# Performance work log

Measured on AMD Instinct MI355X. Metric: run time of the kernel, lower is better.

## Reference

```python
import jax, jax.numpy as jnp
import numpy as np
from jax import lax

EPS = 1e-5

def _conv(x, w, stride, padding):
    # x: NCHW, w: OIHW
    return lax.conv_general_dilated(
        x, w, window_strides=(stride, stride), padding=padding,
        dimension_numbers=("NCHW", "OIHW", "NCHW"))

def _bn(x, gamma, beta):
    # BatchNorm2d in training mode: batch statistics over (N, H, W)
    mean = jnp.mean(x, axis=(0, 2, 3), keepdims=True)
    var = jnp.var(x, axis=(0, 2, 3), keepdims=True)
    inv = lax.rsqrt(var + EPS)
    g = gamma.reshape(1, -1, 1, 1)
    b = beta.reshape(1, -1, 1, 1)
    return (x - mean) * inv * g + b

def setup_inputs() -> dict:
    key = jax.random.key(0)
    ks = jax.random.split(key, 5)
    B, Cin, H, W = 128, 64, 56, 56
    Cout = 128
    x = jax.random.normal(ks[0], (B, Cin, H, W), dtype=jnp.float32)
    w1 = jax.random.normal(ks[1], (Cout, Cin, 3, 3), dtype=jnp.float32) * 0.05
    w2 = jax.random.normal(ks[2], (Cout, Cout, 3, 3), dtype=jnp.float32) * 0.05
    wd = jax.random.normal(ks[3], (Cout, Cin, 1, 1), dtype=jnp.float32) * 0.05
    g1 = jnp.ones((Cout,), jnp.float32); b1 = jnp.zeros((Cout,), jnp.float32)
    g2 = jnp.ones((Cout,), jnp.float32); b2 = jnp.zeros((Cout,), jnp.float32)
    gd = jnp.ones((Cout,), jnp.float32); bd = jnp.zeros((Cout,), jnp.float32)
    return {"x": x, "w1": w1, "g1": g1, "b1": b1,
            "w2": w2, "g2": g2, "b2": b2,
            "wd": wd, "gd": gd, "bd": bd}

def reference(x, w1, g1, b1, w2, g2, b2, wd, gd, bd):
    stride = 2
    # conv1 (3x3, stride=2, 'same') -> BN -> ReLU
    out = _conv(x, w1, stride, "SAME")
    out = jax.nn.relu(_bn(out, g1, b1))
    # conv2 (3x3, stride=1, 'same') -> BN
    out = _conv(out, w2, 1, "SAME")
    out = _bn(out, g2, b2)
    # downsample identity: 1x1 conv stride=2 'valid' -> BN
    identity = _bn(_conv(x, wd, stride, "VALID"), gd, bd)
    return jax.nn.relu(out + identity)
```

## Files before the change

### kernel.cpp

```cpp
#include <hip/hip_runtime.h>

constexpr int B = 128, Cin = 64, H = 56, W = 56;
constexpr int Cout = 128, Ho = 28, Wo = 28;
constexpr int HW = Ho * Wo;
constexpr int NPIX = B * HW;
constexpr int NOUT = NPIX * Cout;
constexpr int NBLK = NPIX / 128;
constexpr float EPS_ = 1e-5f;
constexpr float CNT_ = (float)NPIX;

constexpr int HPX = 57, WPX = 57;
constexpr int HP1 = 30, WP1 = 30;

typedef __attribute__((ext_vector_type(8))) unsigned short u16x8;
typedef __attribute__((ext_vector_type(4))) unsigned short u16x4;
typedef __attribute__((ext_vector_type(8))) short bf16x8;
typedef __attribute__((ext_vector_type(4))) float f32x4;

__device__ inline float bf2f(unsigned short u) {
    union { unsigned int i; float f; } v; v.i = ((unsigned int)u) << 16; return v.f;
}
__device__ inline unsigned short f2bf(float f) {
    union { float f; unsigned int i; } v; v.f = f;
    return (unsigned short)((v.i + 0x7fffu + ((v.i >> 16) & 1u)) >> 16);
}

__device__ inline void gload16(const void* g, void* l) {
    __builtin_amdgcn_global_load_lds(
        (const __attribute__((address_space(1))) unsigned int*)g,
        (__attribute__((address_space(3))) unsigned int*)l, 16, 0, 0);
}

template<int STRIDE, int HP, int WP, int CIN, int KHW, bool OUTPAD, bool FUSE_DW>
__global__ __launch_bounds__(256) void k_conv_mfma(
        const unsigned short* __restrict__ xin,
        const unsigned short* __restrict__ wt,
        unsigned short* __restrict__ yout,
        float* __restrict__ part,
        const unsigned short* __restrict__ wtd,
        unsigned short* __restrict__ ydout,
        float* __restrict__ partd) {
    constexpr int KTOT = KHW * KHW * CIN;
    constexpr int NSTEP = KTOT / 32;
    constexpr int CSTEPS = CIN / 32;
    constexpr int RING = FUSE_DW ? 2 : 3;
    __shared__ unsigned short Alds[RING][128 * 32];
    __shared__ unsigned short Blds[RING][128 * 32];
    __shared__ unsigned short BdLds[FUSE_DW ? 2 * 128 * 32 : 4];
    __shared__ float lsum[4][64], lsq[4][64];
    const int tid = threadIdx.x, w = tid >> 6, l = tid & 63;
    const int wr = w >> 1, wc = w & 1;
    const int bid = (blockIdx.x & 7) * (NBLK / 8) + (blockIdx.x >> 3);
    const int p0 = bid * 128;
    const char* xb = (const char*)xin;
    const char* wb = (const char*)wt;
    const char* wdb = (const char*)wtd;

    const int sslot = ((l & 3) ^ ((l >> 3) & 3)) * 16;
    int gA[2], gB[2], gBd[2], lofs[2];
    #pragma unroll
    for (int i = 0; i < 2; ++i) {
        int row = w * 32 + i * 16 + (l >> 2);
        int p = p0 + row;
        int n = p / HW, rr = p % HW;
        int oh = rr / Wo, ow = rr % Wo;
        gA[i] = (((n * HP + oh * STRIDE) * WP + ow * STRIDE) * CIN) * 2 + sslot;
        gB[i] = (row * KTOT) * 2 + sslot;
        gBd[i] = row * 128 + sslot;
        lofs[i] = row * 64 + (l & 3) * 16;
    }

    f32x4 acc[4][4], accd[4][4];
    #pragma unroll
    for (int m = 0; m < 4; ++m)
        #pragma unroll
        for (int n = 0; n < 4; ++n) {
            acc[m][n] = (f32x4){0.f, 0.f, 0.f, 0.f};
            if constexpr (FUSE_DW) accd[m][n] = (f32x4){0.f, 0.f, 0.f, 0.f};
        }

    auto STAGE = [&](int s, int buf) {
        const int seg = s / CSTEPS;
        const int c0 = (s % CSTEPS) * 32;
        const int kh = seg / KHW, kw = seg % KHW;
        const int koffA = (((kh * WP + kw) * CIN) + c0) * 2;
        const int koffB = s * 64;
        gload16(xb + gA[0] + koffA, (char*)Alds[buf] + lofs[0]);
        gload16(xb + gA[1] + koffA, (char*)Alds[buf] + lofs[1]);
        gload16(wb + gB[0] + koffB, (char*)Blds[buf] + lofs[0]);
        gload16(wb + gB[1] + koffB, (char*)Blds[buf] + lofs[1]);
    };

    const int rswz = ((l >> 4) ^ ((l >> 1) & 3)) * 16;

    if constexpr (FUSE_DW) {
        #pragma unroll
        for (int s = 0; s < 2; ++s)
            #pragma unroll
            for (int i = 0; i < 2; ++i)
                gload16(wdb + gBd[i] + s * 64, (char*)BdLds + s * 8192 + lofs[i]);
    }
    STAGE(0, 0);
    if constexpr (!FUSE_DW) STAGE(1, 1);

    for (int s = 0; s < NSTEP; ++s) {
        const int cur = s % RING;
        if constexpr (FUSE_DW) {
            if (s + 1 < NSTEP) {
                STAGE(s + 1, (s + 1) % RING);
                asm volatile("s_waitcnt vmcnt(4)" ::: "memory");
            } else {
                asm volatile("s_waitcnt vmcnt(0)" ::: "memory");
            }
        } else {
            if (s + 2 < NSTEP) {
                STAGE(s + 2, (s + 2) % RING);
                asm volatile("s_waitcnt vmcnt(8)" ::: "memory");
            } else if (s + 1 < NSTEP) {
                asm volatile("s_waitcnt vmcnt(4)" ::: "memory");
            } else {
                asm volatile("s_waitcnt vmcnt(0)" ::: "memory");
            }
        }
        __builtin_amdgcn_s_barrier();
        bf16x8 af[4], bf[4];
        #pragma unroll
        for (int m = 0; m < 4; ++m)
            af[m] = *(const bf16x8*)((const char*)Alds[cur] + (wr * 64 + m * 16 + (l & 15)) * 64 + rswz);
        #pragma unroll
        for (int n = 0; n < 4; ++n)
            bf[n] = *(const bf16x8*)((const char*)Blds[cur] + (wc * 64 + n * 16 + (l & 15)) * 64 + rswz);
        #pragma unroll
        for (int m = 0; m < 4; ++m)
            #pragma unroll
            for (int n = 0; n < 4; ++n)
                acc[m][n] = __builtin_amdgcn_mfma_f32_16x16x32_bf16(af[m], bf[n], acc[m][n], 0, 0, 0);
        if constexpr (FUSE_DW) {
            if (s < CSTEPS) {
                bf16x8 bd[4];
                #pragma unroll
                for (int n = 0; n < 4; ++n)
                    bd[n] = *(const bf16x8*)((const char*)BdLds + s * 8192 + (wc * 64 + n * 16 + (l & 15)) * 64 + rswz);
                #pragma unroll
                for (int m = 0; m < 4; ++m)
                    #pragma unroll
                    for (int n = 0; n < 4; ++n)
                        accd[m][n] = __builtin_amdgcn_mfma_f32_16x16x32_bf16(af[m], bd[n], accd[m][n], 0, 0, 0);
            }
        }
        __builtin_amdgcn_s_barrier();
    }

    auto store_nchw = [&](f32x4 (&a)[4][4], unsigned short* yo) {
        #pragma unroll
        for (int m = 0; m < 4; ++m) {
            int pq = p0 + wr * 64 + m * 16 + (l >> 4) * 4;
            int n = pq / HW, rr = pq % HW;
            #pragma unroll
            for (int q = 0; q < 4; ++q) {
                int co = wc * 64 + q * 16 + (l & 15);
                u16x4 v;
                #pragma unroll
                for (int r = 0; r < 4; ++r) v[r] = f2bf(a[m][q][r]);
                *(u16x4*)(yo + ((size_t)(n * Cout + co)) * HW + rr) = v;
            }
        }
    };
    auto do_part = [&](f32x4 (&a)[4][4], float* pt) {
        float ps[4], pq_[4];
        #pragma unroll
        for (int n = 0; n < 4; ++n) {
            float s_ = 0.f, q_ = 0.f;
            #pragma unroll
            for (int m = 0; m < 4; ++m)
                #pragma unroll
                for (int r = 0; r < 4; ++r) { float v = a[m][n][r]; s_ += v; q_ += v * v; }
            s_ += __shfl_xor(s_, 16); q_ += __shfl_xor(q_, 16);
            s_ += __shfl_xor(s_, 32); q_ += __shfl_xor(q_, 32);
            ps[n] = s_; pq_[n] = q_;
        }
        __syncthreads();
        if (l < 16) {
            #pragma unroll
            for (int n = 0; n < 4; ++n) { lsum[w][n * 16 + l] = ps[n]; lsq[w][n * 16 + l] = pq_[n]; }
        }
        __syncthreads();
        if (tid < 128) {
            int c = tid, half = c >> 6, j = c & 63;
            pt[((size_t)bid * 128 + c) * 2]     = lsum[half][j] + lsum[half + 2][j];
            pt[((size_t)bid * 128 + c) * 2 + 1] = lsq[half][j] + lsq[half + 2][j];
        }
    };

    if constexpr (OUTPAD) {
        #pragma unroll
        for (int m = 0; m < 4; ++m) {
            #pragma unroll
            for (int r = 0; r < 4; ++r) {
                int p = p0 + wr * 64 + m * 16 + (l >> 4) * 4 + r;
                int n = p / HW, rr = p % HW;
                int oh = rr / Wo, ow = rr % Wo;
                unsigned short* dst = yout + ((size_t)((n * HP1 + oh + 1) * WP1 + ow + 1)) * 128
                                     + wc * 64 + (l & 15);
                #pragma unroll
                for (int q = 0; q < 4; ++q)
                    dst[q * 16] = f2bf(acc[m][q][r]);
            }
        }
    } else {
        store_nchw(acc, yout);
    }
    do_part(acc, part);
    if constexpr (FUSE_DW) {
        store_nchw(accd, ydout);
        do_part(accd, partd);
    }
}

__global__ __launch_bounds__(256) void k_zerob(unsigned short* __restrict__ xb,
                                               unsigned short* __restrict__ y1p) {
    int idx = blockIdx.x * 256 + threadIdx.x;
    constexpr int NA = B * 113 * 8;
    const u16x8 z = (u16x8){0, 0, 0, 0, 0, 0, 0, 0};
    if (idx < NA) {
        int cg = idx & 7; int t = idx >> 3;
        int bp = t % 113, n = t / 113;
        int ih = bp < 57 ? 56 : bp - 57;
        int iw = bp < 57 ? bp : 56;
        *(u16x8*)(xb + ((size_t)((n * HPX + ih) * WPX + iw)) * Cin + cg * 8) = z;
    } else {
        idx -= NA;
        if (idx >= B * 116 * 16) return;
        int cg = idx & 15; int t = idx >> 4;
        int bp = t % 116, n = t / 116;
        int oh, ow;
        if (bp < 30)      { oh = 0;           ow = bp; }
        else if (bp < 60) { oh = 29;          ow = bp - 30; }
        else if (bp < 88) { oh = bp - 60 + 1; ow = 0; }
        else              { oh = bp - 88 + 1; ow = 29; }
        *(u16x8*)(y1p + ((size_t)((n * HP1 + oh) * WP1 + ow)) * 128 + cg * 8) = z;
    }
}

__global__ __launch_bounds__(256) void k_xprep(const float* __restrict__ x,
                                               unsigned short* __restrict__ xb) {
    __shared__ unsigned short lds[64 * 57];
    int n = blockIdx.x / H, ih = blockIdx.x % H;
    const float* src = x + ((size_t)n * Cin * H + ih) * W;
    for (int j = threadIdx.x; j < Cin * W; j += 256) {
        int c = j / W, iw = j % W;
        lds[c * 57 + iw] = f2bf(src[(size_t)c * H * W + iw]);
    }
    __syncthreads();
    unsigned short* dst = xb + ((size_t)(n * HPX + ih)) * WPX * Cin;
    for (int k = threadIdx.x; k < W * 8; k += 256) {
        int pix = k >> 3, cg = k & 7;
        u16x8 v;
        #pragma unroll
        for (int e = 0; e < 8; ++e) v[e] = lds[(cg * 8 + e) * 57 + pix];
        *(u16x8*)(dst + pix * Cin + cg * 8) = v;
    }
}

__global__ void k_wprep_all(const float* __restrict__ w1, const float* __restrict__ w2,
                            const float* __restrict__ wd,
                            unsigned short* __restrict__ wt1, unsigned short* __restrict__ wt2,
                            unsigned short* __restrict__ wtd) {
    int idx = blockIdx.x * 256 + threadIdx.x;
    const float* w; unsigned short* wt; int cin, ntap;
    if (idx < 73728)            { w = w1; wt = wt1; cin = 64;  ntap = 9; }
    else if (idx < 73728 + 147456) { idx -= 73728; w = w2; wt = wt2; cin = 128; ntap = 9; }
    else if (idx < 73728 + 147456 + 8192) { idx -= 73728 + 147456; w = wd; wt = wtd; cin = 64; ntap = 1; }
    else return;
    int co = idx / (cin * ntap), r = idx % (cin * ntap);
    int ci = r / ntap, tap = r % ntap;
    wt[co * cin * ntap + tap * cin + ci] = f2bf(w[idx]);
}

__device__ inline void block_reduce2(float& s, float& s2) {
    #pragma unroll
    for (int off = 32; off > 0; off >>= 1) {
        s += __shfl_down(s, off);
        s2 += __shfl_down(s2, off);
    }
    __shared__ float ls[4], ls2[4];
    int wid = threadIdx.x >> 6, lane = threadIdx.x & 63;
    if (lane == 0) { ls[wid] = s; ls2[wid] = s2; }
    __syncthreads();
    if (threadIdx.x == 0) { s = ls[0] + ls[1] + ls[2] + ls[3]; s2 = ls2[0] + ls2[1] + ls2[2] + ls2[3]; }
}

__global__ __launch_bounds__(256) void k_finalize(
        const float* __restrict__ pA, const float* __restrict__ pB,
        const float* __restrict__ gA, const float* __restrict__ bA,
        const float* __restrict__ gB, const float* __restrict__ bB,
        float* __restrict__ scA, float* __restrict__ shA,
        float* __restrict__ scB, float* __restrict__ shB) {
    const bool second = blockIdx.x >= 128;
    const int c = blockIdx.x & 127;
    const float* part = second ? pB : pA;
    const float* g = second ? gB : gA;
    const float* b = second ? bB : bA;
    float* scale = second ? scB : scA;
    float* shift = second ? shB : shA;
    float s = 0.f, q = 0.f;
    for (int k = threadIdx.x; k < NBLK; k += 256) {
        s += part[((size_t)k * 128 + c) * 2];
        q += part[((size_t)k * 128 + c) * 2 + 1];
    }
    block_reduce2(s, q);
    if (threadIdx.x == 0) {
        float mean = s / CNT_;
        float var = q / CNT_ - mean * mean;
        float inv = rsqrtf(var + EPS_);
        scale[c] = g[c] * inv;
        shift[c] = b[c] - mean * g[c] * inv;
    }
}

__global__ __launch_bounds__(256) void k_bnrelu(unsigned short* __restrict__ y,
        const float* __restrict__ sc, const float* __restrict__ sh) {
    int t = threadIdx.x, cg = t & 15, pl = t >> 4;
    int p = blockIdx.x * 16 + pl;
    int n = p / HW, rr = p % HW;
    int oh = rr / Wo, ow = rr % Wo;
    size_t a = ((size_t)((n * HP1 + oh + 1) * WP1 + ow + 1)) * 128 + cg * 8;
    u16x8 v = *(u16x8*)(y + a);
    u16x8 o;
    #pragma unroll
    for (int e = 0; e < 8; ++e) {
        float f = bf2f(v[e]) * sc[cg * 8 + e] + sh[cg * 8 + e];
        o[e] = f2bf(fmaxf(f, 0.f));
    }
    *(u16x8*)(y + a) = o;
}

__global__ __launch_bounds__(256) void k_final(
        const unsigned short* __restrict__ y2, const unsigned short* __restrict__ yd,
        const float* __restrict__ sc2, const float* __restrict__ sh2,
        const float* __restrict__ scd, const float* __restrict__ shd,
        float* __restrict__ out) {
    int idx = blockIdx.x * 256 + threadIdx.x;
    int plane = idx / (HW / 8);
    int c = plane & (Cout - 1);
    int i = idx % (HW / 8);
    size_t a = (size_t)plane * HW + i * 8;
    u16x8 v2 = *(const u16x8*)(y2 + a);
    u16x8 vd = *(const u16x8*)(yd + a);
    float s2c = sc2[c], h2c = sh2[c], sdc = scd[c], hdc = shd[c];
    float4 r0, r1;
    r0.x = fmaxf(bf2f(v2[0]) * s2c + h2c + bf2f(vd[0]) * sdc + hdc, 0.f);
    r0.y = fmaxf(bf2f(v2[1]) * s2c + h2c + bf2f(vd[1]) * sdc + hdc, 0.f);
    r0.z = fmaxf(bf2f(v2[2]) * s2c + h2c + bf2f(vd[2]) * sdc + hdc, 0.f);
    r0.w = fmaxf(bf2f(v2[3]) * s2c + h2c + bf2f(vd[3]) * sdc + hdc, 0.f);
    r1.x = fmaxf(bf2f(v2[4]) * s2c + h2c + bf2f(vd[4]) * sdc + hdc, 0.f);
    r1.y = fmaxf(bf2f(v2[5]) * s2c + h2c + bf2f(vd[5]) * sdc + hdc, 0.f);
    r1.z = fmaxf(bf2f(v2[6]) * s2c + h2c + bf2f(vd[6]) * sdc + hdc, 0.f);
    r1.w = fmaxf(bf2f(v2[7]) * s2c + h2c + bf2f(vd[7]) * sdc + hdc, 0.f);
    *(float4*)(out + a) = r0;
    *(float4*)(out + a + 4) = r1;
}

extern "C" void kernel_launch(void* const* d_in, const int* in_sizes, int n_in,
                              void* d_out, int out_size, void* d_ws, size_t ws_size,
                              hipStream_t stream) {
    const float* x  = (const float*)d_in[0];
    const float* w1 = (const float*)d_in[1];
    const float* g1 = (const float*)d_in[2];
    const float* b1 = (const float*)d_in[3];
    const float* w2 = (const float*)d_in[4];
    const float* g2 = (const float*)d_in[5];
    const float* b2 = (const float*)d_in[6];
    const float* wd = (const float*)d_in[7];
    const float* gd = (const float*)d_in[8];
    const float* bd = (const float*)d_in[9];
    float* out = (float*)d_out;

    char* ws = (char*)d_ws;
    auto alloc = [&](size_t bytes) { char* p = ws; ws += (bytes + 255) & ~(size_t)255; return p; };
    unsigned short* xb  = (unsigned short*)alloc((size_t)B * HPX * WPX * Cin * 2);
    unsigned short* y1p = (unsigned short*)alloc((size_t)B * HP1 * WP1 * Cout * 2);
    unsigned short* y2b = (unsigned short*)alloc((size_t)NOUT * 2);
    unsigned short* ydb = (unsigned short*)alloc((size_t)NOUT * 2);
    unsigned short* wt1 = (unsigned short*)alloc((size_t)Cout * 576 * 2);
    unsigned short* wt2 = (unsigned short*)alloc((size_t)Cout * 1152 * 2);
    unsigned short* wtd = (unsigned short*)alloc((size_t)Cout * 64 * 2);
    float* part1 = (float*)alloc((size_t)NBLK * 128 * 2 * 4);
    float* part2 = (float*)alloc((size_t)NBLK * 128 * 2 * 4);
    float* partd = (float*)alloc((size_t)NBLK * 128 * 2 * 4);
    float* sc1 = (float*)alloc(128 * 4); float* sh1 = (float*)alloc(128 * 4);
    float* sc2 = (float*)alloc(128 * 4); float* sh2 = (float*)alloc(128 * 4);
    float* scd = (float*)alloc(128 * 4); float* shd = (float*)alloc(128 * 4);

    k_zerob<<<(B * 113 * 8 + B * 116 * 16 + 255) / 256, 256, 0, stream>>>(xb, y1p);
    k_xprep<<<B * H, 256, 0, stream>>>(x, xb);
    k_wprep_all<<<(73728 + 147456 + 8192 + 255) / 256, 256, 0, stream>>>(w1, w2, wd, wt1, wt2, wtd);

    k_conv_mfma<2, HPX, WPX, 64, 3, true, true><<<NBLK, 256, 0, stream>>>(
        xb, wt1, y1p, part1, wtd, ydb, partd);

    k_finalize<<<128, 256, 0, stream>>>(part1, part1, g1, b1, g1, b1, sc1, sh1, sc1, sh1);
    k_bnrelu<<<NPIX / 16, 256, 0, stream>>>(y1p, sc1, sh1);

    k_conv_mfma<1, HP1, WP1, 128, 3, false, false><<<NBLK, 256, 0, stream>>>(
        y1p, wt2, y2b, part2, nullptr, nullptr, nullptr);

    k_finalize<<<256, 256, 0, stream>>>(part2, partd, g2, b2, gd, bd, sc2, sh2, scd, shd);

    k_final<<<NOUT / 8 / 256, 256, 0, stream>>>(y2b, ydb, sc2, sh2, scd, shd, out);
}
```

Measured before the change: 187.6 us.

## Add dedicated 256x128-tile conv2 kernel with 512 threads and block swizzle

Replaces the generic templated conv2 launch with a specialized kernel that computes a 256-pixel by 128-channel tile using 8 waves, each doing a 4x4 grid of 16x16x32 bf16 MFMAs, fed by a 3-deep LDS ring loaded with global_load_lds. Larger tiles halve the number of blocks and increase reuse of the weight tile. The block index is remapped across groups of eight to improve cache locality. The BN-statistics partials now use the halved block count, so the finalize kernel takes the per-input block counts as parameters. The trade-offs are more LDS and register pressure per block and fewer blocks to fill the GPU.

```diff
diff --git a/kernel.cpp b/kernel.cpp
--- a/kernel.cpp
+++ b/kernel.cpp
@@ -6,6 +6,7 @@
 constexpr int NPIX = B * HW;
 constexpr int NOUT = NPIX * Cout;
 constexpr int NBLK = NPIX / 128;
+constexpr int NBLK2 = NPIX / 256;
 constexpr float EPS_ = 1e-5f;
 constexpr float CNT_ = (float)NPIX;
 
@@ -29,6 +30,129 @@
     __builtin_amdgcn_global_load_lds(
         (const __attribute__((address_space(1))) unsigned int*)g,
         (__attribute__((address_space(3))) unsigned int*)l, 16, 0, 0);
+}
+
+__global__ __launch_bounds__(512) void k_conv2_mfma(
+        const unsigned short* __restrict__ xin,
+        const unsigned short* __restrict__ wt,
+        unsigned short* __restrict__ yout,
+        float* __restrict__ part) {
+    constexpr int CIN = 128, WP = 30, KTOT = 1152, NSTEP = 36;
+    __shared__ unsigned short Alds[3][256 * 32];
+    __shared__ unsigned short Blds[3][128 * 32];
+    __shared__ float lsum[8][64], lsq[8][64];
+    const int tid = threadIdx.x, w = tid >> 6, l = tid & 63;
+    const int wr = w >> 1, wc = w & 1;
+    const int bid = (blockIdx.x & 7) * (NBLK2 / 8) + (blockIdx.x >> 3);
+    const int p0 = bid * 256;
+    const char* xb = (const char*)xin;
+    const char* wb = (const char*)wt;
+
+    const int sslot = ((l & 3) ^ ((l >> 3) & 3)) * 16;
+    const int rswz  = ((l >> 4) ^ ((l >> 1) & 3)) * 16;
+
+    int gA[2], lofsA[2];
+    #pragma unroll
+    for (int i = 0; i < 2; ++i) {
+        int row = w * 32 + i * 16 + (l >> 2);
+        int p = p0 + row;
+        int n = p / HW, rr = p % HW;
+        int oh = rr / Wo, ow = rr % Wo;
+        gA[i] = (((n * HP1 + oh) * WP + ow) * CIN) * 2 + sslot;
+        lofsA[i] = row * 64 + (l & 3) * 16;
+    }
+    const int rowb = w * 16 + (l >> 2);
+    const int gB = rowb * KTOT * 2 + sslot;
+    const int lofsB = rowb * 64 + (l & 3) * 16;
+
+    f32x4 acc[4][4];
+    #pragma unroll
+    for (int m = 0; m < 4; ++m)
+        #pragma unroll
+        for (int n = 0; n < 4; ++n)
+            acc[m][n] = (f32x4){0.f, 0.f, 0.f, 0.f};
+
+    gload16(xb + gA[0],      (char*)Alds[0] + lofsA[0]);
+    gload16(xb + gA[1],      (char*)Alds[0] + lofsA[1]);
+    gload16(wb + gB,         (char*)Blds[0] + lofsB);
+    gload16(xb + gA[0] + 64, (char*)Alds[1] + lofsA[0]);
+    gload16(xb + gA[1] + 64, (char*)Alds[1] + lofsA[1]);
+    gload16(wb + gB + 64,    (char*)Blds[1] + lofsB);
+
+    for (int oi = 0; oi < 3; ++oi) {
+        const int Abase = oi * WP * CIN * 2;
+        #pragma unroll
+        for (int u = 0; u < 12; ++u) {
+            const int s = oi * 12 + u;
+            const int cur = u % 3;
+            if (s + 1 < NSTEP) asm volatile("s_waitcnt vmcnt(3)" ::: "memory");
+            else               asm volatile("s_waitcnt vmcnt(0)" ::: "memory");
+            __builtin_amdgcn_s_barrier();
+            if (s + 2 < NSTEP) {
+                const int u2 = u + 2;
+                const int j2 = u2 >> 2;
+                const int c2 = u2 & 3;
+                const int koffA = Abase + (j2 == 3 ? WP * CIN * 2 : j2 * CIN * 2) + c2 * 64;
+                const int koffB = (s + 2) * 64;
+                const int buf = u2 % 3;
+                gload16(xb + gA[0] + koffA, (char*)Alds[buf] + lofsA[0]);
+                gload16(xb + gA[1] + koffA, (char*)Alds[buf] + lofsA[1]);
+                gload16(wb + gB + koffB,    (char*)Blds[buf] + lofsB);
+            }
+            bf16x8 bf[4];
+            #pragma unroll
+            for (int n = 0; n < 4; ++n)
+                bf[n] = *(const bf16x8*)((const char*)Blds[cur] + (wc * 64 + n * 16 + (l & 15)) * 64 + rswz);
+            #pragma unroll
+            for (int m = 0; m < 4; ++m) {
+                bf16x8 af = *(const bf16x8*)((const char*)Alds[cur] + (wr * 64 + m * 16 + (l & 15)) * 64 + rswz);
+                #pragma unroll
+                for (int n = 0; n < 4; ++n)
+                    acc[m][n] = __builtin_amdgcn_mfma_f32_16x16x32_bf16(af, bf[n], acc[m][n], 0, 0, 0);
+            }
+        }
+    }
+
+    #pragma unroll
+    for (int m = 0; m < 4; ++m) {
+        int pq = p0 + wr * 64 + m * 16 + (l >> 4) * 4;
+        int n = pq / HW, rr = pq % HW;
+        #pragma unroll
+        for (int q = 0; q < 4; ++q) {
+            int co = wc * 64 + q * 16 + (l & 15);
+            u16x4 v;
+            #pragma unroll
+            for (int r = 0; r < 4; ++r) v[r] = f2bf(acc[m][q][r]);
+            *(u16x4*)(yout + ((size_t)(n * Cout + co)) * HW + rr) = v;
+        }
+    }
+
+    float ps[4], pq_[4];
+    #pragma unroll
+    for (int n = 0; n < 4; ++n) {
+        float s_ = 0.f, q_ = 0.f;
+        #pragma unroll
+        for (int m = 0; m < 4; ++m)
+            #pragma unroll
+            for (int r = 0; r < 4; ++r) { float v = acc[m][n][r]; s_ += v; q_ += v * v; }
+        s_ += __shfl_xor(s_, 16); q_ += __shfl_xor(q_, 16);
+        s_ += __shfl_xor(s_, 32); q_ += __shfl_xor(q_, 32);
+        ps[n] = s_; pq_[n] = q_;
+    }
+    __syncthreads();
+    if (l < 16) {
+        #pragma unroll
+        for (int n = 0; n < 4; ++n) { lsum[w][n * 16 + l] = ps[n]; lsq[w][n * 16 + l] = pq_[n]; }
+    }
+    __syncthreads();
+    if (tid < 128) {
+        int c = tid, half = c >> 6, j = c & 63;
+        float s_ = 0.f, q_ = 0.f;
+        #pragma unroll
+        for (int r = 0; r < 4; ++r) { s_ += lsum[r * 2 + half][j]; q_ += lsq[r * 2 + half][j]; }
+        part[((size_t)bid * 128 + c) * 2]     = s_;
+        part[((size_t)bid * 128 + c) * 2 + 1] = q_;
+    }
 }
 
 template<int STRIDE, int HP, int WP, int CIN, int KHW, bool OUTPAD, bool FUSE_DW>
@@ -291,20 +415,21 @@
 }
 
 __global__ __launch_bounds__(256) void k_finalize(
-        const float* __restrict__ pA, const float* __restrict__ pB,
-        const float* __restrict__ gA, const float* __restrict__ bA,
-        const float* __restrict__ gB, const float* __restrict__ bB,
+        const float* __restrict__ pA, const float* __restrict__ pB, int nA, int nB,
+        const float* __restrict__ gA_, const float* __restrict__ bA_,
+        const float* __restrict__ gB_, const float* __restrict__ bB_,
         float* __restrict__ scA, float* __restrict__ shA,
         float* __restrict__ scB, float* __restrict__ shB) {
     const bool second = blockIdx.x >= 128;
     const int c = blockIdx.x & 127;
     const float* part = second ? pB : pA;
-    const float* g = second ? gB : gA;
-    const float* b = second ? bB : bA;
+    const int nblk = second ? nB : nA;
+    const float* g = second ? gB_ : gA_;
+    const float* b = second ? bB_ : bA_;
     float* scale = second ? scB : scA;
     float* shift = second ? shB : shA;
     float s = 0.f, q = 0.f;
-    for (int k = threadIdx.x; k < NBLK; k += 256) {
+    for (int k = threadIdx.x; k < nblk; k += 256) {
         s += part[((size_t)k * 128 + c) * 2];
         q += part[((size_t)k * 128 + c) * 2 + 1];
     }
@@ -386,7 +511,7 @@
     unsigned short* wt2 = (unsigned short*)alloc((size_t)Cout * 1152 * 2);
     unsigned short* wtd = (unsigned short*)alloc((size_t)Cout * 64 * 2);
     float* part1 = (float*)alloc((size_t)NBLK * 128 * 2 * 4);
-    float* part2 = (float*)alloc((size_t)NBLK * 128 * 2 * 4);
+    float* part2 = (float*)alloc((size_t)NBLK2 * 128 * 2 * 4);
     float* partd = (float*)alloc((size_t)NBLK * 128 * 2 * 4);
     float* sc1 = (float*)alloc(128 * 4); float* sh1 = (float*)alloc(128 * 4);
     float* sc2 = (float*)alloc(128 * 4); float* sh2 = (float*)alloc(128 * 4);
@@ -399,13 +524,14 @@
     k_conv_mfma<2, HPX, WPX, 64, 3, true, true><<<NBLK, 256, 0, stream>>>(
         xb, wt1, y1p, part1, wtd, ydb, partd);
 
-    k_finalize<<<128, 256, 0, stream>>>(part1, part1, g1, b1, g1, b1, sc1, sh1, sc1, sh1);
+    k_finalize<<<128, 256, 0, stream>>>(part1, part1, NBLK, NBLK,
+                                        g1, b1, g1, b1, sc1, sh1, sc1, sh1);
     k_bnrelu<<<NPIX / 16, 256, 0, stream>>>(y1p, sc1, sh1);
 
-    k_conv_mfma<1, HP1, WP1, 128, 3, false, false><<<NBLK, 256, 0, stream>>>(
-        y1p, wt2, y2b, part2, nullptr, nullptr, nullptr);
-
-    k_finalize<<<256, 256, 0, stream>>>(part2, partd, g2, b2, gd, bd, sc2, sh2, scd, shd);
+    k_conv2_mfma<<<NBLK2, 512, 0, stream>>>(y1p, wt2, y2b, part2);
+
+    k_finalize<<<256, 256, 0, stream>>>(part2, partd, NBLK2, NBLK,
+                                        g2, b2, gd, bd, sc2, sh2, scd, shd);
 
     k_final<<<NOUT / 8 / 256, 256, 0, stream>>>(y2b, ydb, sc2, sh2, scd, shd, out);
 }
```

Result: faster. 175.4 us (-6.5%).
